# Kernel optimization log

Hardware: AMD Instinct MI355X
Metric: run time of the kernel (lower is better)

The kernel has to match this reference:

```python
import jax, jax.numpy as jnp
import numpy as np
import math

N_HEAD = 16
HEAD_DIM = 64  # n_embd // n_head = 1024 / 16
N_EMBD = 1024
B, T = 4, 4096
LIN_K = 1024


def setup_inputs() -> dict:
    key = jax.random.key(0)
    ks = jax.random.split(key, 7)
    s = 0.02
    return {
        "x": jax.random.normal(ks[0], (B, T, N_EMBD), dtype=jnp.float32),
        "W_attn": jax.random.normal(ks[1], (N_EMBD, 3 * N_EMBD), dtype=jnp.float32) * s,
        "b_attn": jax.random.normal(ks[2], (3 * N_EMBD,), dtype=jnp.float32) * s,
        "W_proj": jax.random.normal(ks[3], (N_EMBD, N_EMBD), dtype=jnp.float32) * s,
        "b_proj": jax.random.normal(ks[4], (N_EMBD,), dtype=jnp.float32) * s,
        "E": jax.random.normal(ks[5], (T, LIN_K), dtype=jnp.float32) * s,
        "F": jax.random.normal(ks[6], (T, LIN_K), dtype=jnp.float32) * s,
    }


def reference(x, W_attn, b_attn, W_proj, b_proj, E, F):
    Bb, Tt, C = x.shape
    qkv = x @ W_attn + b_attn                      # (B, T, 3C)
    q, k, v = jnp.split(qkv, 3, axis=-1)
    def heads(t):  # (B, T, C) -> (B, H, T, d)
        return t.reshape(Bb, Tt, N_HEAD, HEAD_DIM).transpose(0, 2, 1, 3)
    q, k, v = heads(q), heads(k), heads(v)
    # Linformer low-rank projection of K and V along the sequence axis
    k_proj = jnp.einsum('bhtd,tk->bhkd', k, E)     # (B, H, K, d)
    v_proj = jnp.einsum('bhtd,tk->bhkd', v, F)
    att = jnp.einsum('bhtd,bhkd->bhtk', q, k_proj) / math.sqrt(HEAD_DIM)
    # causal mask: position t may attend to projected slot j iff j <= t
    mask = jnp.arange(LIN_K)[None, :] <= jnp.arange(Tt)[:, None]  # (T, K)
    att = jnp.where(mask[None, None, :, :], att, -jnp.inf)
    att = jax.nn.softmax(att, axis=-1)
    y = jnp.einsum('bhtk,bhkd->bhtd', att, v_proj)
    y = y.transpose(0, 2, 1, 3).reshape(Bb, Tt, C)
    return y @ W_proj + b_proj
```

## Files before the change

kernel.cpp:

```cpp
#include <hip/hip_runtime.h>
#include <stdint.h>

typedef short bf16x8 __attribute__((ext_vector_type(8)));
typedef short bf16x4 __attribute__((ext_vector_type(4)));
typedef float f32x4 __attribute__((ext_vector_type(4)));
typedef float f32x16 __attribute__((ext_vector_type(16)));
typedef int i32x4 __attribute__((ext_vector_type(4)));

__device__ __forceinline__ short f2bf(float f) {
  union { float f; uint32_t u; } v; v.f = f;
  uint32_t r = (v.u + 0x7FFFu + ((v.u >> 16) & 1u)) >> 16;
  return (short)(uint16_t)r;
}

__device__ __forceinline__ int cvtpk(float lo, float hi) {
  int r;
  asm("v_cvt_pk_bf16_f32 %0, %1, %2" : "=v"(r) : "v"(lo), "v"(hi));
  return r;
}

__device__ __forceinline__ void gload16(const void* g, void* l) {
  __builtin_amdgcn_global_load_lds(
      (const __attribute__((address_space(1))) unsigned int*)g,
      (__attribute__((address_space(3))) unsigned int*)l, 16, 0, 0);
}

#define WAITV(n) asm volatile("s_waitcnt vmcnt(" #n ")" ::: "memory")
#define BARRIER()                          \
  do {                                     \
    __builtin_amdgcn_s_barrier();          \
    asm volatile("" ::: "memory");         \
  } while (0)

__global__ __launch_bounds__(256) void k_cvt_tr(const float* __restrict__ in,
                                                short* __restrict__ xb,
                                                short* __restrict__ xT) {
  __shared__ short tile[32][34];
  const int b = blockIdx.z;
  const int t0 = blockIdx.y * 32, c0 = blockIdx.x * 32;
  const int tx = threadIdx.x & 31, ty = threadIdx.x >> 5;
  const float* src = in + ((size_t)b * 4096 + t0) * 1024 + c0;
  short* dstA = xb + ((size_t)b * 4096 + t0) * 1024 + c0;
#pragma unroll
  for (int j = 0; j < 4; ++j) {
    int r = ty + j * 8;
    short bv = f2bf(src[(size_t)r * 1024 + tx]);
    dstA[(size_t)r * 1024 + tx] = bv;
    tile[tx][r] = bv;
  }
  __syncthreads();
  short* dstT = xT + ((size_t)b * 1024 + c0) * 4096 + t0;
#pragma unroll
  for (int j = 0; j < 4; ++j) {
    int c = ty + j * 8;
    dstT[(size_t)c * 4096 + tx] = tile[c][tx];
  }
}

__global__ __launch_bounds__(256) void k_transpose_cvt(const float* __restrict__ in,
                                                       short* __restrict__ out,
                                                       int R, int C) {
  __shared__ float tile[32][33];
  int r0 = blockIdx.y * 32, c0 = blockIdx.x * 32;
  int tx = threadIdx.x & 31, ty = threadIdx.x >> 5;
#pragma unroll
  for (int j = 0; j < 4; ++j)
    tile[ty + j * 8][tx] = in[(size_t)(r0 + ty + j * 8) * C + c0 + tx];
  __syncthreads();
#pragma unroll
  for (int j = 0; j < 4; ++j)
    out[(size_t)(c0 + ty + j * 8) * R + r0 + tx] = f2bf(tile[tx][ty + j * 8]);
}

__global__ __launch_bounds__(256) void k_colsum1(const float* __restrict__ E,
                                                 const float* __restrict__ F,
                                                 float* __restrict__ partial) {
  const int c = blockIdx.x * 256 + threadIdx.x;
  const int tc = blockIdx.y, which = blockIdx.z;
  const float* src = (which ? F : E) + (size_t)(tc * 64) * 1024 + c;
  float s = 0.f;
#pragma unroll 8
  for (int t = 0; t < 64; ++t) s += src[(size_t)t * 1024];
  partial[((size_t)which * 64 + tc) * 1024 + c] = s;
}

__global__ __launch_bounds__(256) void k_colsum2(const float* __restrict__ partial,
                                                 float* __restrict__ sE,
                                                 float* __restrict__ sF) {
  const int bid = blockIdx.x;
  const int which = bid >> 2, c = (bid & 3) * 256 + threadIdx.x;
  const float* p = partial + (size_t)which * 64 * 1024 + c;
  float s = 0.f;
#pragma unroll 8
  for (int t = 0; t < 64; ++t) s += p[(size_t)t * 1024];
  (which ? sF : sE)[c] = s;
}

__global__ __launch_bounds__(512, 2) void k_gemm_q(const short* __restrict__ A,
                                                   const short* __restrict__ BT,
                                                   const float* __restrict__ bias,
                                                   short* __restrict__ qb) {
  __shared__ __align__(16) char lds[4 * 32768];
  const int tid = threadIdx.x, l = tid & 63, wv = tid >> 6;
  const int wm = wv >> 2, wn = wv & 3;
  const int r16 = l & 15, g4 = l >> 4;
  const int orig = blockIdx.x;
  const int xcd = orig & 7, loc = orig >> 3;
  const int m0 = (xcd * 8 + (loc & 7)) * 256, n0 = (loc >> 3) * 256;
  const int sl = (tid & 3) ^ ((tid >> 3) & 3);
  const short* aS = A + (size_t)(m0 + (tid >> 2)) * 1024 + sl * 8;
  const short* bS = BT + (size_t)(n0 + (tid >> 2)) * 1024 + sl * 8;
  const int sw = (g4 ^ ((r16 >> 1) & 3)) * 16;

  f32x4 acc[8][4];
#pragma unroll
  for (int i = 0; i < 8; ++i)
#pragma unroll
    for (int j = 0; j < 4; ++j) acc[i][j] = f32x4{0.f, 0.f, 0.f, 0.f};

#define STAGEQ(kt, bf)                                                      \
  {                                                                         \
    const int k0_ = (kt) * 32;                                              \
    gload16(aS + k0_, lds + (bf) * 32768 + tid * 16);                       \
    gload16(aS + 131072 + k0_, lds + (bf) * 32768 + 8192 + tid * 16);       \
    gload16(bS + k0_, lds + (bf) * 32768 + 16384 + tid * 16);               \
    gload16(bS + 131072 + k0_, lds + (bf) * 32768 + 24576 + tid * 16);      \
  }

  STAGEQ(0, 0); STAGEQ(1, 1); STAGEQ(2, 2);

  for (int kt = 0; kt < 32; ++kt) {
    if (kt < 30) WAITV(8);
    else if (kt == 30) WAITV(4);
    else WAITV(0);
    BARRIER();
    if (kt + 3 < 32) STAGEQ(kt + 3, (kt + 3) & 3);
    const char* aT = lds + (kt & 3) * 32768;
    const char* bT = aT + 16384;
    bf16x8 af[8], bfr[4];
#pragma unroll
    for (int mi = 0; mi < 8; ++mi)
      af[mi] = *(const bf16x8*)(aT + (wm * 128 + mi * 16 + r16) * 64 + sw);
#pragma unroll
    for (int ni = 0; ni < 4; ++ni)
      bfr[ni] = *(const bf16x8*)(bT + (wn * 64 + ni * 16 + r16) * 64 + sw);
    __builtin_amdgcn_s_setprio(1);
#pragma unroll
    for (int mi = 0; mi < 8; ++mi)
#pragma unroll
      for (int ni = 0; ni < 4; ++ni)
        acc[mi][ni] = __builtin_amdgcn_mfma_f32_16x16x32_bf16(af[mi], bfr[ni], acc[mi][ni], 0, 0, 0);
    __builtin_amdgcn_s_setprio(0);
  }
#undef STAGEQ

#pragma unroll
  for (int i = 0; i < 8; ++i)
#pragma unroll
    for (int j = 0; j < 4; ++j) {
      int row = m0 + wm * 128 + i * 16 + g4 * 4;
      int col = n0 + wn * 64 + j * 16 + r16;
      float bv = bias[col];
#pragma unroll
      for (int q = 0; q < 4; ++q)
        qb[(size_t)(row + q) * 1024 + col] = f2bf(acc[i][j][q] + bv);
    }
}

__global__ __launch_bounds__(512, 2) void k_proj(const short* __restrict__ Et,
                                                 const short* __restrict__ Ft,
                                                 const short* __restrict__ xT,
                                                 short* __restrict__ xEk,
                                                 short* __restrict__ xEv) {
  const int z = blockIdx.z, b = z >> 1, which = z & 1;
  const short* __restrict__ AT = which ? Ft : Et;
  const short* __restrict__ BTp = xT + ((size_t)b << 10) * 4096;
  short* __restrict__ outp = which ? xEv : xEk;
  __shared__ __align__(16) char lds[3 * 24576];
  const int tid = threadIdx.x, l = tid & 63, wv = tid >> 6;
  const int wm = wv >> 1, wn = wv & 1;
  const int r16 = l & 15, g4 = l >> 4;
  const int m0 = blockIdx.x * 256, n0 = blockIdx.y * 128;
  const int sl = (tid & 3) ^ ((tid >> 3) & 3);
  const short* aS = AT + (size_t)(m0 + (tid >> 2)) * 4096 + sl * 8;
  const short* bS = BTp + (size_t)(n0 + (tid >> 2)) * 4096 + sl * 8;
  const int sw = (g4 ^ ((r16 >> 1) & 3)) * 16;

  f32x4 acc[4][4];
#pragma unroll
  for (int i = 0; i < 4; ++i)
#pragma unroll
    for (int j = 0; j < 4; ++j) acc[i][j] = f32x4{0.f, 0.f, 0.f, 0.f};

#define STAGE2(kt, bf)                                                      \
  {                                                                         \
    const int k0_ = (kt) * 32;                                              \
    gload16(aS + k0_, lds + (bf) * 24576 + tid * 16);                       \
    gload16(aS + 524288 + k0_, lds + (bf) * 24576 + 8192 + tid * 16);       \
    gload16(bS + k0_, lds + (bf) * 24576 + 16384 + tid * 16);               \
  }

  STAGE2(0, 0); STAGE2(1, 1);

  for (int kt = 0; kt < 128; ++kt) {
    if (kt < 127) WAITV(3);
    else WAITV(0);
    BARRIER();
    if (kt + 2 < 128) STAGE2(kt + 2, (kt + 2) % 3);
    const char* aT = lds + (kt % 3) * 24576;
    const char* bT = aT + 16384;
    bf16x8 af[4], bfr[4];
#pragma unroll
    for (int mi = 0; mi < 4; ++mi)
      af[mi] = *(const bf16x8*)(aT + (wm * 64 + mi * 16 + r16) * 64 + sw);
#pragma unroll
    for (int ni = 0; ni < 4; ++ni)
      bfr[ni] = *(const bf16x8*)(bT + (wn * 64 + ni * 16 + r16) * 64 + sw);
    __builtin_amdgcn_s_setprio(1);
#pragma unroll
    for (int mi = 0; mi < 4; ++mi)
#pragma unroll
      for (int ni = 0; ni < 4; ++ni)
        acc[mi][ni] = __builtin_amdgcn_mfma_f32_16x16x32_bf16(af[mi], bfr[ni], acc[mi][ni], 0, 0, 0);
    __builtin_amdgcn_s_setprio(0);
  }
#undef STAGE2

#pragma unroll
  for (int i = 0; i < 4; ++i)
#pragma unroll
    for (int j = 0; j < 4; ++j) {
      int row = m0 + wm * 64 + i * 16 + g4 * 4;
      int col = n0 + wn * 64 + j * 16 + r16;
#pragma unroll
      for (int q = 0; q < 4; ++q)
        outp[((size_t)(b * 1024) + row + q) * 1024 + col] = f2bf(acc[i][j][q]);
    }
}

__global__ __launch_bounds__(256, 2) void k_kpvp(const short* __restrict__ xEk,
                                                 const short* __restrict__ xEv,
                                                 const short* __restrict__ WaT,
                                                 const float* __restrict__ b_attn,
                                                 const float* __restrict__ sE,
                                                 const float* __restrict__ sF,
                                                 short* __restrict__ kp,
                                                 short* __restrict__ vpt) {
  const int which = blockIdx.z;
  const short* __restrict__ A = which ? xEv : xEk;
  const short* __restrict__ BT = WaT + (size_t)(1024 + which * 1024) * 1024;
  const float* __restrict__ bias = b_attn + 1024 + which * 1024;
  const float* __restrict__ rs = which ? sF : sE;
  __shared__ __align__(16) char lds[4 * 16384];
  const int tid = threadIdx.x, l = tid & 63, wv = tid >> 6;
  const int wm = wv >> 1, wn = wv & 1;
  const int r16 = l & 15, g4 = l >> 4;
  const int m0 = blockIdx.x * 128, n0 = blockIdx.y * 128;
  const int sl = (tid & 3) ^ ((tid >> 3) & 3);
  const short* aS = A + (size_t)(m0 + (tid >> 2)) * 1024 + sl * 8;
  const short* bS = BT + (size_t)(n0 + (tid >> 2)) * 1024 + sl * 8;
  const int sw = (g4 ^ ((r16 >> 1) & 3)) * 16;

  f32x4 acc[4][4];
#pragma unroll
  for (int i = 0; i < 4; ++i)
#pragma unroll
    for (int j = 0; j < 4; ++j) acc[i][j] = f32x4{0.f, 0.f, 0.f, 0.f};

#define STAGEP(kt, bf)                                                      \
  {                                                                         \
    const int k0_ = (kt) * 32;                                              \
    gload16(aS + k0_, lds + (bf) * 16384 + tid * 16);                       \
    gload16(aS + 65536 + k0_, lds + (bf) * 16384 + 4096 + tid * 16);        \
    gload16(bS + k0_, lds + (bf) * 16384 + 8192 + tid * 16);                \
    gload16(bS + 65536 + k0_, lds + (bf) * 16384 + 12288 + tid * 16);       \
  }

  STAGEP(0, 0); STAGEP(1, 1); STAGEP(2, 2);

  for (int kt = 0; kt < 32; ++kt) {
    if (kt < 30) WAITV(8);
    else if (kt == 30) WAITV(4);
    else WAITV(0);
    BARRIER();
    if (kt + 3 < 32) STAGEP(kt + 3, (kt + 3) & 3);
    const char* aT = lds + (kt & 3) * 16384;
    const char* bT = aT + 8192;
    bf16x8 af[4], bfr[4];
#pragma unroll
    for (int mi = 0; mi < 4; ++mi)
      af[mi] = *(const bf16x8*)(aT + (wm * 64 + mi * 16 + r16) * 64 + sw);
#pragma unroll
    for (int ni = 0; ni < 4; ++ni)
      bfr[ni] = *(const bf16x8*)(bT + (wn * 64 + ni * 16 + r16) * 64 + sw);
    __builtin_amdgcn_s_setprio(1);
#pragma unroll
    for (int mi = 0; mi < 4; ++mi)
#pragma unroll
      for (int ni = 0; ni < 4; ++ni)
        acc[mi][ni] = __builtin_amdgcn_mfma_f32_16x16x32_bf16(af[mi], bfr[ni], acc[mi][ni], 0, 0, 0);
    __builtin_amdgcn_s_setprio(0);
  }
#undef STAGEP

  if (which) {
#pragma unroll
    for (int i = 0; i < 4; ++i)
#pragma unroll
      for (int j = 0; j < 4; ++j) {
        int row = m0 + wm * 64 + i * 16 + g4 * 4;
        int col = n0 + wn * 64 + j * 16 + r16;
        int bb = row >> 10;
        float bv = bias[col];
        bf16x4 ov;
#pragma unroll
        for (int q = 0; q < 4; ++q)
          ov[q] = f2bf(acc[i][j][q] + rs[(row + q) & 1023] * bv);
        *reinterpret_cast<bf16x4*>(
            &vpt[(((size_t)bb << 10) + col) * 1024 + (row & 1023)]) = ov;
      }
  } else {
    const float KSCALE = 0.125f * 1.4426950408889634f;
#pragma unroll
    for (int i = 0; i < 4; ++i)
#pragma unroll
      for (int j = 0; j < 4; ++j) {
        int row = m0 + wm * 64 + i * 16 + g4 * 4;
        int col = n0 + wn * 64 + j * 16 + r16;
        float bv = bias[col];
#pragma unroll
        for (int q = 0; q < 4; ++q)
          kp[(size_t)(row + q) * 1024 + col] =
              f2bf((acc[i][j][q] + rs[(row + q) & 1023] * bv) * KSCALE);
      }
  }
}

__global__ __launch_bounds__(256, 3) void k_attn(const short* __restrict__ qb,
                                                 const short* __restrict__ kp,
                                                 const short* __restrict__ vpt,
                                                 short* __restrict__ y) {
  __shared__ __align__(16) char KsB[128 * 128];
  __shared__ __align__(16) char VtB[64 * 256];
  const int tid = threadIdx.x, lane = tid & 63, w = tid >> 6;
  const int r32 = lane & 31, hi = lane >> 5;
  const int iblk = 31 - blockIdx.x;
  const int bh = blockIdx.y, b = bh >> 4, h = bh & 15;
  const int t0 = iblk * 128;
  const int tl = w * 32 + r32;
  const int T = t0 + tl;

  bf16x8 qf[4];
#pragma unroll
  for (int kd = 0; kd < 4; ++kd)
    qf[kd] = *reinterpret_cast<const bf16x8*>(
        &qb[(size_t)(b * 4096 + T) * 1024 + h * 64 + kd * 16 + hi * 8]);

  f32x16 o[2];
#pragma unroll
  for (int i = 0; i < 16; ++i) { o[0][i] = 0.f; o[1][i] = 0.f; }
  float lrun = 0.f;

  const short* kpb = kp + ((size_t)b << 20) + h * 64;
  const short* vtb = vpt + (((size_t)b << 10) + h * 64) * 1024;

  const int kkl_ = tid >> 3, c8 = tid & 7;
  const int dl_ = tid >> 4, c16 = tid & 15;
  bf16x8 kreg[4], vreg[4];

#define LOADT(jt)                                                              \
  {                                                                            \
    const int kk0_ = (jt) * 128;                                               \
    _Pragma("unroll") for (int it = 0; it < 4; ++it) {                         \
      kreg[it] = *reinterpret_cast<const bf16x8*>(                             \
          &kpb[(size_t)(kk0_ + it * 32 + kkl_) * 1024 + c8 * 8]);              \
      vreg[it] = *reinterpret_cast<const bf16x8*>(                             \
          &vtb[(size_t)(it * 16 + dl_) * 1024 + kk0_ + c16 * 8]);              \
    }                                                                          \
  }

  LOADT(0);

  const int ntiles = (iblk + 1 < 8) ? (iblk + 1) : 8;
  for (int jt = 0; jt < ntiles; ++jt) {
    WAITV(0);
    BARRIER();
#pragma unroll
    for (int it = 0; it < 4; ++it) {
      int kk = it * 32 + kkl_;
      *reinterpret_cast<bf16x8*>(&KsB[kk * 128 + ((c8 * 16) ^ ((kk & 7) << 4))]) = kreg[it];
      int d = it * 16 + dl_;
      *reinterpret_cast<bf16x8*>(&VtB[d * 256 + ((c16 * 16) ^ ((d & 7) << 4))]) = vreg[it];
    }
    __syncthreads();
    if (jt + 1 < ntiles) LOADT(jt + 1);

#pragma unroll
    for (int st = 0; st < 2; ++st) {
      f32x16 s[2];
#pragma unroll
      for (int i = 0; i < 16; ++i) { s[0][i] = 0.f; s[1][i] = 0.f; }
#pragma unroll
      for (int ni = 0; ni < 2; ++ni) {
        int row = (st * 2 + ni) * 32 + r32;
#pragma unroll
        for (int kd = 0; kd < 4; ++kd) {
          bf16x8 kf = *reinterpret_cast<const bf16x8*>(
              &KsB[row * 128 + ((kd * 32 + hi * 16) ^ ((row & 7) << 4))]);
          s[ni] = __builtin_amdgcn_mfma_f32_32x32x16_bf16(kf, qf[kd], s[ni], 0, 0, 0);
        }
      }

      if (jt == iblk) {
#pragma unroll
        for (int ni = 0; ni < 2; ++ni)
#pragma unroll
          for (int j = 0; j < 16; ++j) {
            int kkl = (st * 2 + ni) * 32 + (j & 3) + 8 * (j >> 2) + 4 * hi;
            if (kkl > tl) s[ni][j] = -1e30f;
          }
      }

      float r0 = 0.f, r1 = 0.f, r2 = 0.f, r3 = 0.f;
#pragma unroll
      for (int j = 0; j < 16; j += 2) {
        float e0 = __builtin_amdgcn_exp2f(s[0][j]);
        float e1 = __builtin_amdgcn_exp2f(s[0][j + 1]);
        float e2 = __builtin_amdgcn_exp2f(s[1][j]);
        float e3 = __builtin_amdgcn_exp2f(s[1][j + 1]);
        s[0][j] = e0; s[0][j + 1] = e1; s[1][j] = e2; s[1][j + 1] = e3;
        r0 += e0; r1 += e1; r2 += e2; r3 += e3;
      }
      float rsum = (r0 + r1) + (r2 + r3);
      rsum += __shfl_xor(rsum, 32, 64);
      lrun += rsum;

#pragma unroll
      for (int kbl = 0; kbl < 4; ++kbl) {
        const int ni = kbl >> 1, jb = (kbl & 1) * 8;
        int lo0 = cvtpk(s[ni][jb + 0], s[ni][jb + 1]);
        int lo1 = cvtpk(s[ni][jb + 2], s[ni][jb + 3]);
        int hi0 = cvtpk(s[ni][jb + 4], s[ni][jb + 5]);
        int hi1 = cvtpk(s[ni][jb + 6], s[ni][jb + 7]);
        asm("v_permlane32_swap_b32 %0, %1" : "+v"(lo0), "+v"(hi0));
        asm("v_permlane32_swap_b32 %0, %1" : "+v"(lo1), "+v"(hi1));
        i32x4 pw; pw[0] = lo0; pw[1] = lo1; pw[2] = hi0; pw[3] = hi1;
        bf16x8 pf = __builtin_bit_cast(bf16x8, pw);
        const int kb = st * 4 + kbl;
#pragma unroll
        for (int mo = 0; mo < 2; ++mo) {
          int row = mo * 32 + r32;
          bf16x8 vf = *reinterpret_cast<const bf16x8*>(
              &VtB[row * 256 + ((kb * 32 + hi * 16) ^ ((row & 7) << 4))]);
          o[mo] = __builtin_amdgcn_mfma_f32_32x32x16_bf16(vf, pf, o[mo], 0, 0, 0);
        }
      }
    }
  }

  float inv = 1.0f / lrun;
#pragma unroll
  for (int mo = 0; mo < 2; ++mo)
#pragma unroll
    for (int rq = 0; rq < 4; ++rq) {
      bf16x4 ov;
#pragma unroll
      for (int c = 0; c < 4; ++c) ov[c] = f2bf(o[mo][rq * 4 + c] * inv);
      *reinterpret_cast<bf16x4*>(
          &y[(size_t)(b * 4096 + T) * 1024 + h * 64 + mo * 32 + rq * 8 + hi * 4]) = ov;
    }
#undef LOADT
}

__global__ __launch_bounds__(512, 2) void k_gemm_out(const short* __restrict__ A,
                                                     const short* __restrict__ BT,
                                                     const float* __restrict__ bias,
                                                     float* __restrict__ C) {
  __shared__ __align__(16) char lds[4 * 32768];
  const int tid = threadIdx.x, l = tid & 63, wv = tid >> 6;
  const int wm = wv >> 2, wn = wv & 3;
  const int r16 = l & 15, g4 = l >> 4;
  const int orig = blockIdx.x;
  const int xcd = orig & 7, loc = orig >> 3;
  const int m0 = (xcd * 8 + (loc & 7)) * 256, n0 = (loc >> 3) * 256;
  const int sl = (tid & 3) ^ ((tid >> 3) & 3);
  const short* aS = A + (size_t)(m0 + (tid >> 2)) * 1024 + sl * 8;
  const short* bS = BT + (size_t)(n0 + (tid >> 2)) * 1024 + sl * 8;
  const int sw = (g4 ^ ((r16 >> 1) & 3)) * 16;

  f32x4 acc[8][4];
#pragma unroll
  for (int i = 0; i < 8; ++i)
#pragma unroll
    for (int j = 0; j < 4; ++j) acc[i][j] = f32x4{0.f, 0.f, 0.f, 0.f};

#define STAGE3(kt, bf)                                                      \
  {                                                                         \
    const int k0_ = (kt) * 32;                                              \
    gload16(aS + k0_, lds + (bf) * 32768 + tid * 16);                       \
    gload16(aS + 131072 + k0_, lds + (bf) * 32768 + 8192 + tid * 16);       \
    gload16(bS + k0_, lds + (bf) * 32768 + 16384 + tid * 16);               \
    gload16(bS + 131072 + k0_, lds + (bf) * 32768 + 24576 + tid * 16);      \
  }

  STAGE3(0, 0); STAGE3(1, 1); STAGE3(2, 2);

  for (int kt = 0; kt < 32; ++kt) {
    if (kt < 30) WAITV(8);
    else if (kt == 30) WAITV(4);
    else WAITV(0);
    BARRIER();
    if (kt + 3 < 32) STAGE3(kt + 3, (kt + 3) & 3);
    const char* aT = lds + (kt & 3) * 32768;
    const char* bT = aT + 16384;
    bf16x8 af[8], bfr[4];
#pragma unroll
    for (int mi = 0; mi < 8; ++mi)
      af[mi] = *(const bf16x8*)(aT + (wm * 128 + mi * 16 + r16) * 64 + sw);
#pragma unroll
    for (int ni = 0; ni < 4; ++ni)
      bfr[ni] = *(const bf16x8*)(bT + (wn * 64 + ni * 16 + r16) * 64 + sw);
    __builtin_amdgcn_s_setprio(1);
#pragma unroll
    for (int mi = 0; mi < 8; ++mi)
#pragma unroll
      for (int ni = 0; ni < 4; ++ni)
        acc[mi][ni] = __builtin_amdgcn_mfma_f32_16x16x32_bf16(af[mi], bfr[ni], acc[mi][ni], 0, 0, 0);
    __builtin_amdgcn_s_setprio(0);
  }
#undef STAGE3

#pragma unroll
  for (int i = 0; i < 8; ++i)
#pragma unroll
    for (int j = 0; j < 4; ++j) {
      int row = m0 + wm * 128 + i * 16 + g4 * 4;
      int col = n0 + wn * 64 + j * 16 + r16;
      float bv = bias[col];
#pragma unroll
      for (int q = 0; q < 4; ++q)
        C[(size_t)(row + q) * 1024 + col] = acc[i][j][q] + bv;
    }
}

extern "C" void kernel_launch(void* const* d_in, const int* in_sizes, int n_in,
                              void* d_out, int out_size, void* d_ws, size_t ws_size,
                              hipStream_t stream) {
  const float* x      = (const float*)d_in[0];
  const float* W_attn = (const float*)d_in[1];
  const float* b_attn = (const float*)d_in[2];
  const float* W_proj = (const float*)d_in[3];
  const float* b_proj = (const float*)d_in[4];
  const float* E      = (const float*)d_in[5];
  const float* F      = (const float*)d_in[6];
  float* out = (float*)d_out;

  char* ws = (char*)d_ws;
  short* xb  = (short*)(ws + 0);
  short* WaT = (short*)(ws + 33554432);
  short* WpT = (short*)(ws + 39845888);
  short* Et  = (short*)(ws + 41943040);
  short* Ft  = (short*)(ws + 50331648);
  short* qb  = (short*)(ws + 58720256);
  short* xTb = (short*)(ws + 92274688);
  short* xEk = (short*)(ws + 125829120);
  short* xEv = (short*)(ws + 134217728);
  short* kp  = (short*)(ws + 142606336);
  short* vpt = (short*)(ws + 150994944);
  short* yb  = (short*)(ws + 159383552);
  float* sE  = (float*)(ws + 192937984);
  float* sF  = (float*)(ws + 192942080);
  float* part= (float*)(ws + 192946176);

  k_cvt_tr<<<dim3(32, 128, 4), 256, 0, stream>>>(x, xb, xTb);
  k_transpose_cvt<<<dim3(96, 32), 256, 0, stream>>>(W_attn, WaT, 1024, 3072);
  k_transpose_cvt<<<dim3(32, 32), 256, 0, stream>>>(W_proj, WpT, 1024, 1024);
  k_transpose_cvt<<<dim3(32, 128), 256, 0, stream>>>(E, Et, 4096, 1024);
  k_transpose_cvt<<<dim3(32, 128), 256, 0, stream>>>(F, Ft, 4096, 1024);
  k_colsum1<<<dim3(4, 64, 2), 256, 0, stream>>>(E, F, part);
  k_colsum2<<<8, 256, 0, stream>>>(part, sE, sF);

  k_gemm_q<<<256, 512, 0, stream>>>(xb, WaT, b_attn, qb);
  k_proj<<<dim3(4, 8, 8), 512, 0, stream>>>(Et, Ft, xTb, xEk, xEv);
  k_kpvp<<<dim3(32, 8, 2), 256, 0, stream>>>(xEk, xEv, WaT, b_attn, sE, sF, kp, vpt);
  k_attn<<<dim3(32, 64), 256, 0, stream>>>(qb, kp, vpt, yb);
  k_gemm_out<<<256, 512, 0, stream>>>(yb, WpT, b_proj, out);
}
```

Baseline: 321.5 us.

## Process two 128-row query groups per attention block to reuse K/V tiles

Each attention workgroup now handles 256 query rows (two 128-row groups) instead of 128, so every K/V tile staged into shared memory feeds twice the MFMA work. The grid halves, and the first group's compute is placed before the next tile's global load is issued. The cost is more registers (two sets of Q fragments and output accumulators), which drops launch bounds occupancy from 3 to 2 waves-per-SIMD blocks, and fewer blocks in the grid.

```diff
diff --git a/kernel.cpp b/kernel.cpp
--- a/kernel.cpp
+++ b/kernel.cpp
@@ -336,7 +336,7 @@
   }
 }
 
-__global__ __launch_bounds__(256, 3) void k_attn(const short* __restrict__ qb,
+__global__ __launch_bounds__(256, 2) void k_attn(const short* __restrict__ qb,
                                                  const short* __restrict__ kp,
                                                  const short* __restrict__ vpt,
                                                  short* __restrict__ y) {
@@ -344,22 +344,25 @@
   __shared__ __align__(16) char VtB[64 * 256];
   const int tid = threadIdx.x, lane = tid & 63, w = tid >> 6;
   const int r32 = lane & 31, hi = lane >> 5;
-  const int iblk = 31 - blockIdx.x;
+  const int iblk = 15 - blockIdx.x;
   const int bh = blockIdx.y, b = bh >> 4, h = bh & 15;
-  const int t0 = iblk * 128;
+  const int t0 = iblk * 256;
   const int tl = w * 32 + r32;
-  const int T = t0 + tl;
-
-  bf16x8 qf[4];
-#pragma unroll
-  for (int kd = 0; kd < 4; ++kd)
-    qf[kd] = *reinterpret_cast<const bf16x8*>(
-        &qb[(size_t)(b * 4096 + T) * 1024 + h * 64 + kd * 16 + hi * 8]);
-
-  f32x16 o[2];
-#pragma unroll
-  for (int i = 0; i < 16; ++i) { o[0][i] = 0.f; o[1][i] = 0.f; }
-  float lrun = 0.f;
+
+  bf16x8 qf[2][4];
+#pragma unroll
+  for (int rg = 0; rg < 2; ++rg)
+#pragma unroll
+    for (int kd = 0; kd < 4; ++kd)
+      qf[rg][kd] = *reinterpret_cast<const bf16x8*>(
+          &qb[(size_t)(b * 4096 + t0 + rg * 128 + tl) * 1024 + h * 64 + kd * 16 + hi * 8]);
+
+  f32x16 o[2][2];
+#pragma unroll
+  for (int rg = 0; rg < 2; ++rg)
+#pragma unroll
+    for (int i = 0; i < 16; ++i) { o[rg][0][i] = 0.f; o[rg][1][i] = 0.f; }
+  float lr0 = 0.f, lr1 = 0.f;
 
   const short* kpb = kp + ((size_t)b << 20) + h * 64;
   const short* vtb = vpt + (((size_t)b << 10) + h * 64) * 1024;
@@ -379,9 +382,62 @@
     }                                                                          \
   }
 
+#define ATT_RG(RG, LRUN)                                                       \
+  {                                                                            \
+    f32x16 s[2];                                                               \
+    _Pragma("unroll") for (int st = 0; st < 2; ++st) {                         \
+      _Pragma("unroll") for (int i = 0; i < 16; ++i) { s[0][i] = 0.f; s[1][i] = 0.f; } \
+      _Pragma("unroll") for (int ni = 0; ni < 2; ++ni) {                       \
+        int row = (st * 2 + ni) * 32 + r32;                                    \
+        _Pragma("unroll") for (int kd = 0; kd < 4; ++kd) {                     \
+          bf16x8 kf = *reinterpret_cast<const bf16x8*>(                        \
+              &KsB[row * 128 + ((kd * 32 + hi * 16) ^ ((row & 7) << 4))]);     \
+          s[ni] = __builtin_amdgcn_mfma_f32_32x32x16_bf16(kf, qf[RG][kd], s[ni], 0, 0, 0); \
+        }                                                                      \
+      }                                                                        \
+      if (jt == 2 * iblk + RG) {                                               \
+        _Pragma("unroll") for (int ni = 0; ni < 2; ++ni)                       \
+          _Pragma("unroll") for (int j = 0; j < 16; ++j) {                     \
+            int kkl = (st * 2 + ni) * 32 + (j & 3) + 8 * (j >> 2) + 4 * hi;    \
+            if (kkl > tl) s[ni][j] = -1e30f;                                   \
+          }                                                                    \
+      }                                                                        \
+      float r0 = 0.f, r1 = 0.f, r2 = 0.f, r3 = 0.f;                            \
+      _Pragma("unroll") for (int j = 0; j < 16; j += 2) {                      \
+        float e0 = __builtin_amdgcn_exp2f(s[0][j]);                            \
+        float e1 = __builtin_amdgcn_exp2f(s[0][j + 1]);                        \
+        float e2 = __builtin_amdgcn_exp2f(s[1][j]);                            \
+        float e3 = __builtin_amdgcn_exp2f(s[1][j + 1]);                        \
+        s[0][j] = e0; s[0][j + 1] = e1; s[1][j] = e2; s[1][j + 1] = e3;        \
+        r0 += e0; r1 += e1; r2 += e2; r3 += e3;                                \
+      }                                                                        \
+      float rsum = (r0 + r1) + (r2 + r3);                                      \
+      rsum += __shfl_xor(rsum, 32, 64);                                        \
+      LRUN += rsum;                                                            \
+      _Pragma("unroll") for (int kbl = 0; kbl < 4; ++kbl) {                    \
+        const int ni = kbl >> 1, jb = (kbl & 1) * 8;                           \
+        int lo0 = cvtpk(s[ni][jb + 0], s[ni][jb + 1]);                         \
+        int lo1 = cvtpk(s[ni][jb + 2], s[ni][jb + 3]);                         \
+        int hi0 = cvtpk(s[ni][jb + 4], s[ni][jb + 5]);                         \
+        int hi1 = cvtpk(s[ni][jb + 6], s[ni][jb + 7]);                         \
+        asm("v_permlane32_swap_b32 %0, %1" : "+v"(lo0), "+v"(hi0));            \
+        asm("v_permlane32_swap_b32 %0, %1" : "+v"(lo1), "+v"(hi1));            \
+        i32x4 pw; pw[0] = lo0; pw[1] = lo1; pw[2] = hi0; pw[3] = hi1;          \
+        bf16x8 pf = __builtin_bit_cast(bf16x8, pw);                            \
+        const int kb = st * 4 + kbl;                                           \
+        _Pragma("unroll") for (int mo = 0; mo < 2; ++mo) {                     \
+          int row = mo * 32 + r32;                                             \
+          bf16x8 vf = *reinterpret_cast<const bf16x8*>(                        \
+              &VtB[row * 256 + ((kb * 32 + hi * 16) ^ ((row & 7) << 4))]);     \
+          o[RG][mo] = __builtin_amdgcn_mfma_f32_32x32x16_bf16(vf, pf, o[RG][mo], 0, 0, 0); \
+        }                                                                      \
+      }                                                                        \
+    }                                                                          \
+  }
+
   LOADT(0);
 
-  const int ntiles = (iblk + 1 < 8) ? (iblk + 1) : 8;
+  const int ntiles = (2 * iblk + 2 < 8) ? (2 * iblk + 2) : 8;
   for (int jt = 0; jt < ntiles; ++jt) {
     WAITV(0);
     BARRIER();
@@ -393,82 +449,29 @@
       *reinterpret_cast<bf16x8*>(&VtB[d * 256 + ((c16 * 16) ^ ((d & 7) << 4))]) = vreg[it];
     }
     __syncthreads();
+
+    if (jt <= 2 * iblk) ATT_RG(0, lr0);
     if (jt + 1 < ntiles) LOADT(jt + 1);
-
-#pragma unroll
-    for (int st = 0; st < 2; ++st) {
-      f32x16 s[2];
-#pragma unroll
-      for (int i = 0; i < 16; ++i) { s[0][i] = 0.f; s[1][i] = 0.f; }
-#pragma unroll
-      for (int ni = 0; ni < 2; ++ni) {
-        int row = (st * 2 + ni) * 32 + r32;
-#pragma unroll
-        for (int kd = 0; kd < 4; ++kd) {
-          bf16x8 kf = *reinterpret_cast<const bf16x8*>(
-              &KsB[row * 128 + ((kd * 32 + hi * 16) ^ ((row & 7) << 4))]);
-          s[ni] = __builtin_amdgcn_mfma_f32_32x32x16_bf16(kf, qf[kd], s[ni], 0, 0, 0);
-        }
+    ATT_RG(1, lr1);
+  }
+
+#pragma unroll
+  for (int rg = 0; rg < 2; ++rg) {
+    float lr = rg ? lr1 : lr0;
+    float inv = 1.0f / lr;
+    const int T = t0 + rg * 128 + tl;
+#pragma unroll
+    for (int mo = 0; mo < 2; ++mo)
+#pragma unroll
+      for (int rq = 0; rq < 4; ++rq) {
+        bf16x4 ov;
+#pragma unroll
+        for (int c = 0; c < 4; ++c) ov[c] = f2bf(o[rg][mo][rq * 4 + c] * inv);
+        *reinterpret_cast<bf16x4*>(
+            &y[(size_t)(b * 4096 + T) * 1024 + h * 64 + mo * 32 + rq * 8 + hi * 4]) = ov;
       }
-
-      if (jt == iblk) {
-#pragma unroll
-        for (int ni = 0; ni < 2; ++ni)
-#pragma unroll
-          for (int j = 0; j < 16; ++j) {
-            int kkl = (st * 2 + ni) * 32 + (j & 3) + 8 * (j >> 2) + 4 * hi;
-            if (kkl > tl) s[ni][j] = -1e30f;
-          }
-      }
-
-      float r0 = 0.f, r1 = 0.f, r2 = 0.f, r3 = 0.f;
-#pragma unroll
-      for (int j = 0; j < 16; j += 2) {
-        float e0 = __builtin_amdgcn_exp2f(s[0][j]);
-        float e1 = __builtin_amdgcn_exp2f(s[0][j + 1]);
-        float e2 = __builtin_amdgcn_exp2f(s[1][j]);
-        float e3 = __builtin_amdgcn_exp2f(s[1][j + 1]);
-        s[0][j] = e0; s[0][j + 1] = e1; s[1][j] = e2; s[1][j + 1] = e3;
-        r0 += e0; r1 += e1; r2 += e2; r3 += e3;
-      }
-      float rsum = (r0 + r1) + (r2 + r3);
-      rsum += __shfl_xor(rsum, 32, 64);
-      lrun += rsum;
-
-#pragma unroll
-      for (int kbl = 0; kbl < 4; ++kbl) {
-        const int ni = kbl >> 1, jb = (kbl & 1) * 8;
-        int lo0 = cvtpk(s[ni][jb + 0], s[ni][jb + 1]);
-        int lo1 = cvtpk(s[ni][jb + 2], s[ni][jb + 3]);
-        int hi0 = cvtpk(s[ni][jb + 4], s[ni][jb + 5]);
-        int hi1 = cvtpk(s[ni][jb + 6], s[ni][jb + 7]);
-        asm("v_permlane32_swap_b32 %0, %1" : "+v"(lo0), "+v"(hi0));
-        asm("v_permlane32_swap_b32 %0, %1" : "+v"(lo1), "+v"(hi1));
-        i32x4 pw; pw[0] = lo0; pw[1] = lo1; pw[2] = hi0; pw[3] = hi1;
-        bf16x8 pf = __builtin_bit_cast(bf16x8, pw);
-        const int kb = st * 4 + kbl;
-#pragma unroll
-        for (int mo = 0; mo < 2; ++mo) {
-          int row = mo * 32 + r32;
-          bf16x8 vf = *reinterpret_cast<const bf16x8*>(
-              &VtB[row * 256 + ((kb * 32 + hi * 16) ^ ((row & 7) << 4))]);
-          o[mo] = __builtin_amdgcn_mfma_f32_32x32x16_bf16(vf, pf, o[mo], 0, 0, 0);
-        }
-      }
-    }
-  }
-
-  float inv = 1.0f / lrun;
-#pragma unroll
-  for (int mo = 0; mo < 2; ++mo)
-#pragma unroll
-    for (int rq = 0; rq < 4; ++rq) {
-      bf16x4 ov;
-#pragma unroll
-      for (int c = 0; c < 4; ++c) ov[c] = f2bf(o[mo][rq * 4 + c] * inv);
-      *reinterpret_cast<bf16x4*>(
-          &y[(size_t)(b * 4096 + T) * 1024 + h * 64 + mo * 32 + rq * 8 + hi * 4]) = ov;
-    }
+  }
+#undef ATT_RG
 #undef LOADT
 }
 
@@ -583,6 +586,6 @@
   k_gemm_q<<<256, 512, 0, stream>>>(xb, WaT, b_attn, qb);
   k_proj<<<dim3(4, 8, 8), 512, 0, stream>>>(Et, Ft, xTb, xEk, xEv);
   k_kpvp<<<dim3(32, 8, 2), 256, 0, stream>>>(xEk, xEv, WaT, b_attn, sE, sF, kp, vpt);
-  k_attn<<<dim3(32, 64), 256, 0, stream>>>(qb, kp, vpt, yb);
+  k_attn<<<dim3(16, 64), 256, 0, stream>>>(qb, kp, vpt, yb);
   k_gemm_out<<<256, 512, 0, stream>>>(yb, WpT, b_proj, out);
 }
```

After: 321.6 us. Within noise of the previous version (+0.0%).
